# Kernel optimization log

Hardware: AMD Instinct MI355X
Metric: run time of the kernel (lower is better)

The kernel has to match this reference:

```python
import jax, jax.numpy as jnp
import numpy as np
from jax import lax

B, TX, TY = 32, 512, 1024
D, H, FN, KS, L = 256, 2, 1024, 9, 4
WORD_NUM = 256
NEG = -1e9


def sinusoid_table(seq_len, d):
    pos = np.arange(seq_len)[:, None].astype(np.float64)
    i = np.arange(d)[None, :]
    angle = pos / np.power(10000.0, 2 * (i // 2) / d)
    table = np.zeros((seq_len, d))
    table[:, 0::2] = np.sin(angle[:, 0::2])
    table[:, 1::2] = np.cos(angle[:, 1::2])
    return jnp.asarray(table, dtype=jnp.float32)


def setup_inputs():
    key = jax.random.key(0)
    ks = jax.random.split(key, 16)
    s = 0.02
    w = lambda k, shape: jax.random.normal(k, shape, jnp.float32) * s
    embed = w(ks[4], (WORD_NUM, D)).at[0].set(0.0)  # padding_idx=0
    return dict(
        tokens=jax.random.randint(ks[0], (B, TX), 1, WORD_NUM),
        src_lengths=jax.random.randint(ks[1], (B,), TX // 2, TX + 1),
        mel_lengths=jax.random.randint(ks[2], (B,), TY // 2, TY + 1),
        value=jax.random.normal(ks[3], (B, TX, TY), jnp.float32),
        embed=embed,
        pos_enc=sinusoid_table(TX, D),
        wq=w(ks[5], (L, D, D)), bq=jnp.zeros((L, D), jnp.float32),
        wk=w(ks[6], (L, D, D)), bk=jnp.zeros((L, D), jnp.float32),
        wv=w(ks[7], (L, D, D)), bv=jnp.zeros((L, D), jnp.float32),
        wo=w(ks[8], (L, D, D)), bo=jnp.zeros((L, D), jnp.float32),
        ln1_g=jnp.ones((L, D), jnp.float32), ln1_b=jnp.zeros((L, D), jnp.float32),
        c1_w=w(ks[9], (L, FN, D, KS)), c1_b=jnp.zeros((L, FN), jnp.float32),
        c2_w=w(ks[10], (L, D, FN, KS)), c2_b=jnp.zeros((L, D), jnp.float32),
        ln2_g=jnp.ones((L, D), jnp.float32), ln2_b=jnp.zeros((L, D), jnp.float32),
    )


def layer_norm(x, g, b, eps=1e-5):
    m = jnp.mean(x, axis=-1, keepdims=True)
    v = jnp.mean(jnp.square(x - m), axis=-1, keepdims=True)
    return (x - m) * lax.rsqrt(v + eps) * g + b


def conv1d(x, w, b):
    # x: [B, C_in, T], w: [C_out, C_in, K]
    p = (w.shape[-1] - 1) // 2
    y = lax.conv_general_dilated(x, w, (1,), [(p, p)],
                                 dimension_numbers=('NCH', 'OIH', 'NCH'))
    return y + b[None, :, None]


def maximum_path(value, mask):
    # Monotonic alignment search DP. value, mask: [B, Tx, Ty]
    b, tx, ty = value.shape
    value = value * mask
    x_range = jnp.arange(tx)[None, :]

    def fwd_step(v, inp):
        j, val_j = inp
        v0 = jnp.concatenate([jnp.full((b, 1), NEG, value.dtype), v[:, :-1]], axis=1)
        max_mask = v >= v0
        v_max = jnp.where(max_mask, v, v0)
        v_new = jnp.where(x_range <= j, v_max + val_j, NEG)
        return v_new, max_mask

    _, directions = lax.scan(fwd_step, jnp.zeros((b, tx), value.dtype),
                             (jnp.arange(ty), jnp.moveaxis(value, 2, 0)))
    directions = jnp.where(jnp.moveaxis(mask, 2, 0).astype(bool), directions, True)

    idx0 = mask[:, :, 0].sum(1).astype(jnp.int32) - 1  # last valid x index per batch
    brange = jnp.arange(b)

    def bwd_step(idx, dir_j):
        col = jax.nn.one_hot(idx, tx, dtype=value.dtype)
        idx_new = idx + dir_j[brange, idx].astype(jnp.int32) - 1
        return idx_new, col

    _, cols = lax.scan(bwd_step, idx0, directions, reverse=True)
    path = jnp.moveaxis(cols, 0, 2) * mask  # [B, Tx, Ty]
    return path


def reference(tokens, src_lengths, mel_lengths, value, embed, pos_enc,
              wq, bq, wk, bk, wv, bv, wo, bo, ln1_g, ln1_b,
              c1_w, c1_b, c2_w, c2_b, ln2_g, ln2_b):
    bsz, tx = tokens.shape
    pad = jnp.arange(tx)[None, :] >= src_lengths[:, None]      # [B,Tx] True=pad
    mel_pad = jnp.arange(TY)[None, :] >= mel_lengths[:, None]  # [B,Ty]
    dk = D // H
    scale = 1.0 / np.sqrt(dk).astype(np.float32)

    x = embed[tokens] + pos_enc[None, :tx, :]
    for l in range(L):
        # --- multi-head self-attention ---
        res = x
        q = (x @ wq[l] + bq[l]).reshape(bsz, tx, H, dk)
        k = (x @ wk[l] + bk[l]).reshape(bsz, tx, H, dk)
        v = (x @ wv[l] + bv[l]).reshape(bsz, tx, H, dk)
        attn = jnp.einsum('bqhd,bkhd->bhqk', q, k) * scale
        attn = jnp.where(pad[:, None, None, :], NEG, attn)
        attn = jax.nn.softmax(attn, axis=-1)
        out = jnp.einsum('bhqk,bkhd->bqhd', attn, v).reshape(bsz, tx, D)
        x = layer_norm(out @ wo[l] + bo[l] + res, ln1_g[l], ln1_b[l])
        x = jnp.where(pad[:, :, None], 0.0, x)
        # --- conv1d FFN ---
        res = x
        h = x.transpose(0, 2, 1)
        h = jax.nn.relu(conv1d(h, c1_w[l], c1_b[l]))
        h = conv1d(h, c2_w[l], c2_b[l]).transpose(0, 2, 1)
        x = layer_norm(h + res, ln2_g[l], ln2_b[l])
        x = jnp.where(pad[:, :, None], 0.0, x)

    mas_mask = ((~pad)[:, :, None] & (~mel_pad)[:, None, :]).astype(jnp.float32)
    path = maximum_path(value, mas_mask)                 # [B,Tx,Ty]
    expanded = jnp.einsum('bxy,bxd->byd', path, x)       # [B,Ty,D]
    return expanded
```

## Files before the change

kernel.cpp:

```cpp
#include <hip/hip_runtime.h>

#define B_  32
#define TX  512
#define TY  1024
#define D_  256
#define H_  2
#define DK  128
#define FN  1024
#define NL  4
#define TXP 520
#define NEGF (-1e9f)

typedef __attribute__((ext_vector_type(4))) float f32x4;
typedef __attribute__((ext_vector_type(8))) short short8;
typedef __attribute__((ext_vector_type(4))) unsigned short ushort4v;

typedef __attribute__((address_space(3))) unsigned int lds_u32;
typedef __attribute__((address_space(1))) const unsigned int glb_u32;

__device__ __forceinline__ unsigned short f2bf(float x) {
  unsigned int u = __builtin_bit_cast(unsigned int, x);
  u += 0x7fffu + ((u >> 16) & 1u);
  return (unsigned short)(u >> 16);
}
__device__ __forceinline__ float bf2f(unsigned short x) {
  unsigned int u = ((unsigned int)x) << 16;
  return __builtin_bit_cast(float, u);
}
__device__ __forceinline__ void store_bf16x4(unsigned short* p, f32x4 v) {
  ushort4v o; o[0]=f2bf(v[0]); o[1]=f2bf(v[1]); o[2]=f2bf(v[2]); o[3]=f2bf(v[3]);
  *(ushort4v*)p = o;
}
__device__ __forceinline__ float wsum(float v) {
#pragma unroll
  for (int i = 1; i < 64; i <<= 1) v += __shfl_xor(v, i, 64);
  return v;
}
__device__ __forceinline__ float wmax(float v) {
#pragma unroll
  for (int i = 1; i < 64; i <<= 1) v = fmaxf(v, __shfl_xor(v, i, 64));
  return v;
}
__device__ __forceinline__ void gl_lds16(const unsigned short* g, unsigned short* l) {
  __builtin_amdgcn_global_load_lds((glb_u32*)g, (lds_u32*)l, 16, 0, 0);
}
__device__ __forceinline__ float lane_shr1(float x) {
  int r = __builtin_amdgcn_update_dpp(0, __builtin_bit_cast(int, x), 0x138, 0xF, 0xF, false);
  return __builtin_bit_cast(float, r);
}

static const size_t OFF_XB   = 0;
static const size_t SZ_XB    = (size_t)B_*TXP*D_*2;
static const size_t OFF_HB   = OFF_XB + SZ_XB;
static const size_t SZ_HB    = (size_t)B_*TXP*FN*2;
static const size_t OFF_QKV  = OFF_HB + SZ_HB;
static const size_t SZ_QKV   = (size_t)B_*TX*768*2;
static const size_t OFF_S    = OFF_QKV + SZ_QKV;
static const size_t SZ_S     = (size_t)B_*H_*TX*TX*2;
static const size_t OFF_AO   = OFF_S + SZ_S;
static const size_t SZ_AO    = (size_t)B_*TX*D_*2;
static const size_t OFF_T1   = OFF_AO + SZ_AO;
static const size_t SZ_T1    = (size_t)B_*TX*D_*4;
static const size_t OFF_WQKV = OFF_T1 + SZ_T1;
static const size_t SZ_WQKV  = (size_t)NL*768*256*2;
static const size_t OFF_BQKV = OFF_WQKV + SZ_WQKV;
static const size_t SZ_BQKV  = (size_t)NL*768*4;
static const size_t OFF_WO   = OFF_BQKV + SZ_BQKV;
static const size_t SZ_WO    = (size_t)NL*256*256*2;
static const size_t OFF_WT1  = OFF_WO + SZ_WO;
static const size_t SZ_WT1   = (size_t)NL*9*1024*256*2;
static const size_t OFF_WT2  = OFF_WT1 + SZ_WT1;
static const size_t SZ_WT2   = SZ_WT1;
static const size_t OFF_DIRS = OFF_WT2 + SZ_WT2;
static const size_t SZ_DIRS  = (size_t)B_*TY*64;
static const size_t OFF_IDX  = OFF_DIRS + SZ_DIRS;

__global__ void repack_qkvw(const float* __restrict__ wq, const float* __restrict__ wk,
                            const float* __restrict__ wv, unsigned short* __restrict__ out) {
  int i = blockIdx.x*256 + threadIdx.x;
  if (i >= NL*768*256) return;
  int c = i & 255, j = (i >> 8) % 768, l = i / (768*256);
  const float* src = (j < 256) ? wq : (j < 512) ? wk : wv;
  out[i] = f2bf(src[((size_t)l*256 + c)*256 + (j & 255)]);
}
__global__ void repack_bias(const float* __restrict__ bq, const float* __restrict__ bk,
                            const float* __restrict__ bv, float* __restrict__ out) {
  int i = blockIdx.x*256 + threadIdx.x;
  if (i >= NL*768) return;
  int j = i % 768, l = i / 768;
  const float* src = (j < 256) ? bq : (j < 512) ? bk : bv;
  out[i] = src[l*256 + (j & 255)];
}
__global__ void repack_wo(const float* __restrict__ wo, unsigned short* __restrict__ out) {
  int i = blockIdx.x*256 + threadIdx.x;
  if (i >= NL*256*256) return;
  int c = i & 255, j = (i >> 8) & 255, l = i >> 16;
  out[i] = f2bf(wo[((size_t)l*256 + c)*256 + j]);
}
__global__ void repack_c1(const float* __restrict__ w, unsigned short* __restrict__ out) {
  int i = blockIdx.x*256 + threadIdx.x;
  if (i >= NL*9*1024*256) return;
  int c = i & 255; int rest = i >> 8;
  int f = rest & 1023; int rest2 = rest >> 10;
  int k = rest2 % 9, l = rest2 / 9;
  out[i] = f2bf(w[(((size_t)l*1024 + f)*256 + c)*9 + k]);
}
__global__ void repack_c2(const float* __restrict__ w, unsigned short* __restrict__ out) {
  int i = blockIdx.x*256 + threadIdx.x;
  if (i >= NL*9*256*1024) return;
  int f = i & 1023; int rest = i >> 10;
  int d = rest & 255; int rest2 = rest >> 8;
  int k = rest2 % 9, l = rest2 / 9;
  out[i] = f2bf(w[(((size_t)l*256 + d)*1024 + f)*9 + k]);
}
__global__ void zero_halo(unsigned short* __restrict__ xb, unsigned short* __restrict__ hb) {
  int i = blockIdx.x*256 + threadIdx.x;
  if (i < 65536) {
    int b = i >> 11, r = (i >> 8) & 7, c = i & 255;
    int row = (r < 4) ? r : (512 + r);
    xb[((size_t)b*TXP + row)*256 + c] = 0;
  } else {
    int j = i - 65536;
    if (j < 262144) {
      int b = j >> 13, r = (j >> 10) & 7, c = j & 1023;
      int row = (r < 4) ? r : (512 + r);
      hb[((size_t)b*TXP + row)*1024 + c] = 0;
    }
  }
}

__global__ __launch_bounds__(256) void embed_kernel(const int* __restrict__ tok,
    const float* __restrict__ emb, const float* __restrict__ pos,
    unsigned short* __restrict__ xbo ) {
  int row = blockIdx.x*4 + (threadIdx.x >> 6);
  int t = row & 511, b = row >> 9;
  int lane = threadIdx.x & 63;
  int tk = tok[row];
  f32x4 e = *(const f32x4*)(emb + (size_t)tk*256 + lane*4);
  f32x4 p = *(const f32x4*)(pos + (size_t)t*256 + lane*4);
  f32x4 v;
#pragma unroll
  for (int i = 0; i < 4; i++) v[i] = e[i] + p[i];
  store_bf16x4(xbo + ((size_t)b*TXP + t)*256 + lane*4, v);
}

__global__ __launch_bounds__(256) void gemm_mfma(
    const unsigned short* __restrict__ A, long long AbO, long long AhO, int Astr,
    const unsigned short* __restrict__ W, long long WbO, long long WhO, int Wstr,
    const float* __restrict__ bias,
    float* __restrict__ O32, long long O32bO, int O32str,
    unsigned short* __restrict__ O16, long long O16bO, long long O16hO, int O16str,
    int Cin, int Cout, int ks, int relu, int H,
    const int* __restrict__ sl, float scale, int maskmode) {
  __shared__ unsigned short As[128*32];
  __shared__ unsigned short Ws[128*32];
  const int tid = threadIdx.x;
  int b, h;
  if (H == 2) { b = blockIdx.z >> 1; h = blockIdx.z & 1; }
  else        { b = blockIdx.z;      h = 0; }
  const int t0 = blockIdx.x * 128;
  const int f0 = blockIdx.y * 128;
  const unsigned short* Ab = A + (size_t)b * AbO + (size_t)h * AhO;
  const unsigned short* Wb = W + (size_t)b * WbO + (size_t)h * WhO;
  const int lane = tid & 63, w = tid >> 6;
  const int wt = (w & 1) << 6, wf = (w >> 1) << 6;
  const int lr = lane & 15, lh = lane >> 4;
  const int r0 = tid >> 2, cg = (tid & 3) << 3;
  f32x4 zed = {0.f, 0.f, 0.f, 0.f};
  f32x4 acc[4][4];
#pragma unroll
  for (int i = 0; i < 4; i++)
#pragma unroll
    for (int j = 0; j < 4; j++) acc[i][j] = zed;

  for (int k = 0; k < ks; ++k) {
    const unsigned short* AkB = Ab + (size_t)(t0 + k) * Astr;
    const unsigned short* WkB = Wb + ((size_t)k * Cout + f0) * Wstr;
    for (int c0 = 0; c0 < Cin; c0 += 32) {
      __syncthreads();
      gl_lds16(AkB + (size_t)r0 * Astr + (c0 + cg),        As + (size_t)tid * 8);
      gl_lds16(AkB + (size_t)(r0 + 64) * Astr + (c0 + cg), As + (size_t)(tid + 256) * 8);
      gl_lds16(WkB + (size_t)r0 * Wstr + (c0 + cg),        Ws + (size_t)tid * 8);
      gl_lds16(WkB + (size_t)(r0 + 64) * Wstr + (c0 + cg), Ws + (size_t)(tid + 256) * 8);
      __syncthreads();
      short8 af[4], bfv[4];
#pragma unroll
      for (int mt = 0; mt < 4; mt++) af[mt]  = *(const short8*)&As[(wt + mt*16 + lr)*32 + lh*8];
#pragma unroll
      for (int nt = 0; nt < 4; nt++) bfv[nt] = *(const short8*)&Ws[(wf + nt*16 + lr)*32 + lh*8];
#pragma unroll
      for (int mt = 0; mt < 4; mt++)
#pragma unroll
        for (int nt = 0; nt < 4; nt++)
          acc[mt][nt] = __builtin_amdgcn_mfma_f32_16x16x32_bf16(af[mt], bfv[nt], acc[mt][nt], 0, 0, 0);
    }
  }
  const int slb = maskmode ? sl[b] : 0;
#pragma unroll
  for (int mt = 0; mt < 4; mt++) {
    int trow = t0 + wt + mt*16 + lh*4;
#pragma unroll
    for (int nt = 0; nt < 4; nt++) {
      int f = f0 + wf + nt*16 + lr;
      float bb = (!maskmode && bias) ? bias[f] : 0.f;
#pragma unroll
      for (int r = 0; r < 4; r++) {
        float v;
        if (maskmode) {
          v = acc[mt][nt][r] * scale;
          if (f >= slb) v = NEGF;
        } else {
          v = acc[mt][nt][r] + bb;
          if (relu) v = fmaxf(v, 0.f);
        }
        if (O32) O32[(size_t)b*O32bO + (size_t)(trow + r)*O32str + f] = v;
        if (O16) O16[(size_t)b*O16bO + (size_t)h*O16hO + (size_t)(trow + r)*O16str + f] = f2bf(v);
      }
    }
  }
}

__global__ __launch_bounds__(256) void vtrans_kernel(const unsigned short* __restrict__ qkv,
    unsigned short* __restrict__ VT) {
  const int z = blockIdx.z, b = z >> 1, h = z & 1;
  const int t0 = blockIdx.x << 5, d0 = blockIdx.y << 5;
  __shared__ unsigned short tile[32][33];
  const int tx = threadIdx.x, ty = threadIdx.y;
  const unsigned short* src = qkv + (size_t)b*TX*768 + 512 + h*DK;
#pragma unroll
  for (int i = 0; i < 4; i++)
    tile[ty + i*8][tx] = src[(size_t)(t0 + ty + i*8)*768 + d0 + tx];
  __syncthreads();
#pragma unroll
  for (int i = 0; i < 4; i++)
    VT[((size_t)z*DK + d0 + ty + i*8)*512 + t0 + tx] = tile[tx][ty + i*8];
}

__global__ __launch_bounds__(256) void softmax_kernel(unsigned short* __restrict__ S) {
  const int row = blockIdx.x*4 + (threadIdx.x >> 6);
  const int lane = threadIdx.x & 63;
  unsigned short* p = S + (size_t)row*512 + lane*8;
  short8 raw = *(const short8*)p;
  float a[8];
#pragma unroll
  for (int i = 0; i < 8; i++) a[i] = bf2f((unsigned short)raw[i]);
  float m = a[0];
#pragma unroll
  for (int i = 1; i < 8; i++) m = fmaxf(m, a[i]);
  m = wmax(m);
  float s = 0.f;
#pragma unroll
  for (int i = 0; i < 8; i++) { a[i] = __expf(a[i]-m); s += a[i]; }
  s = wsum(s);
  float inv = 1.f / s;
  short8 o;
#pragma unroll
  for (int i = 0; i < 8; i++) o[i] = (short)f2bf(a[i] * inv);
  *(short8*)p = o;
}

__global__ __launch_bounds__(256) void ln_kernel(const float* __restrict__ tin,
    const float* __restrict__ g, const float* __restrict__ bt, const int* __restrict__ sl,
    unsigned short* __restrict__ xbo ) {
  const int row = blockIdx.x*4 + (threadIdx.x >> 6);
  const int b = row >> 9, t = row & 511;
  const int lane = threadIdx.x & 63;
  unsigned short* xp = xbo + ((size_t)b*TXP + t)*256 + lane*4;
  f32x4 tv = *(const f32x4*)(tin + (size_t)row*256 + lane*4);
  ushort4v rv4 = *(const ushort4v*)xp;
  f32x4 s; float su = 0.f, sq = 0.f;
#pragma unroll
  for (int i = 0; i < 4; i++) {
    s[i] = tv[i] + bf2f(rv4[i]);
    su += s[i]; sq += s[i]*s[i];
  }
  su = wsum(su); sq = wsum(sq);
  float mean = su * (1.f/256.f);
  float var = fmaxf(sq * (1.f/256.f) - mean*mean, 0.f);
  float rs = rsqrtf(var + 1e-5f);
  f32x4 gg = *(const f32x4*)(g + lane*4);
  f32x4 bb = *(const f32x4*)(bt + lane*4);
  bool padr = (t >= sl[b]);
  f32x4 y;
#pragma unroll
  for (int i = 0; i < 4; i++) {
    float yy = (s[i]-mean)*rs*gg[i] + bb[i];
    y[i] = padr ? 0.f : yy;
  }
  store_bf16x4(xp, y);
}

__global__ __launch_bounds__(256) void transpose_mask(const float* __restrict__ value,
    const int* __restrict__ sl, const int* __restrict__ ml, float* __restrict__ vT) {
  const int b = blockIdx.z;
  const int x0 = blockIdx.y << 5, y0 = blockIdx.x << 5;
  __shared__ float tile[32][33];
  const int tx = threadIdx.x, ty = threadIdx.y;
  const int slb = sl[b], mlb = ml[b];
#pragma unroll
  for (int i = 0; i < 4; i++) {
    int x = x0 + ty + i*8, y = y0 + tx;
    float v = value[((size_t)b*TX + x)*TY + y];
    tile[ty + i*8][tx] = (x < slb && y < mlb) ? v : 0.f;
  }
  __syncthreads();
#pragma unroll
  for (int i = 0; i < 4; i++) {
    int y = y0 + ty + i*8, x = x0 + tx;
    vT[((size_t)b*TY + y)*TX + x] = tile[tx][ty + i*8];
  }
}

__global__ __launch_bounds__(64, 1) void dp_forward(const float* __restrict__ vT,
    const int* __restrict__ sl, const int* __restrict__ ml, unsigned char* __restrict__ dirs) {
  const int b = blockIdx.x;
  const int lane = threadIdx.x;
  const int slb = sl[b], mlb = ml[b];
  const float* vb = vT + (size_t)b*TY*TX + lane*8;
  unsigned char* db = dirs + (size_t)b*TY*64 + lane;
  const int xbase = lane*8;
  float v[8];
#pragma unroll
  for (int i = 0; i < 8; i++) v[i] = 0.f;
  f32x4 b0[8][2], b1[8][2], b2[8][2];
  auto load8 = [&](int jb, f32x4 (&bf)[8][2]) {
#pragma unroll
    for (int u = 0; u < 8; u++) {
      const float* p = vb + (size_t)(jb*8 + u)*TX;
      bf[u][0] = *(const f32x4*)p;
      bf[u][1] = *(const f32x4*)(p + 4);
    }
  };
  auto comp8 = [&](int jb, f32x4 (&bf)[8][2]) {
#pragma unroll
    for (int u = 0; u < 8; u++) {
      const int j = jb*8 + u;
      float vp = lane_shr1(v[7]);
      if (lane == 0) vp = NEGF;
      float v0[8];
      v0[0] = vp;
#pragma unroll
      for (int i = 1; i < 8; i++) v0[i] = v[i-1];
      unsigned int byt = 0;
#pragma unroll
      for (int i = 0; i < 8; i++) {
        const int x = xbase + i;
        bool ge = (v[i] >= v0[i]);
        bool dbit = (x < slb) ? ge : true;
        byt |= ((unsigned)dbit) << i;
        float vm = fmaxf(v[i], v0[i]);
        float val = (i < 4) ? bf[u][0][i] : bf[u][1][i-4];
        v[i] = (x <= j) ? (vm + val) : NEGF;
      }
      if (j < mlb) db[(size_t)j*64] = (unsigned char)byt;
    }
  };
  const int jbEnd = (mlb + 7) >> 3;
  load8(0, b0);
  __builtin_amdgcn_sched_barrier(0);
  load8(1, b1);
  __builtin_amdgcn_sched_barrier(0);
  load8(2, b2);
  __builtin_amdgcn_sched_barrier(0);
  for (int jb = 0; jb < jbEnd; jb += 3) {
    comp8(jb, b0);
    __builtin_amdgcn_sched_barrier(0);
    if (jb + 3 < jbEnd) { load8(jb + 3, b0); }
    __builtin_amdgcn_sched_barrier(0);
    if (jb + 1 < jbEnd) {
      comp8(jb + 1, b1);
      __builtin_amdgcn_sched_barrier(0);
      if (jb + 4 < jbEnd) { load8(jb + 4, b1); }
      __builtin_amdgcn_sched_barrier(0);
    }
    if (jb + 2 < jbEnd) {
      comp8(jb + 2, b2);
      __builtin_amdgcn_sched_barrier(0);
      if (jb + 5 < jbEnd) { load8(jb + 5, b2); }
      __builtin_amdgcn_sched_barrier(0);
    }
  }
}

__global__ __launch_bounds__(64) void dp_backward(const unsigned char* __restrict__ dirs,
    const int* __restrict__ sl, const int* __restrict__ ml, int* __restrict__ idxout) {
  extern __shared__ unsigned int ldsw[];
  const int b = blockIdx.x, lane = threadIdx.x;
  const unsigned int* src = (const unsigned int*)(dirs + (size_t)b*TY*64);
  for (int i = lane; i < TY*16; i += 64) ldsw[i] = src[i];
  __syncthreads();
  if (lane == 0) {
    int idx = sl[b] - 1;
    const int mlb = ml[b];
    int* ob = idxout + b*TY;
    for (int j = TY - 1; j >= 0; --j) {
      if (j < mlb) {
        ob[j] = idx;
        unsigned int w = ldsw[j*16 + (idx >> 5)];
        idx += (int)((w >> (idx & 31)) & 1u) - 1;
      } else ob[j] = -1;
    }
  }
}

__global__ __launch_bounds__(256) void gather_kernel(const unsigned short* __restrict__ xbo,
    const int* __restrict__ idxout, float* __restrict__ out) {
  const int row = blockIdx.x*4 + (threadIdx.x >> 6);
  const int lane = threadIdx.x & 63;
  const int b = row >> 10;
  const int idx = idxout[row];
  f32x4 v;
  if (idx >= 0) {
    ushort4v r = *(const ushort4v*)(xbo + ((size_t)b*TXP + idx)*256 + lane*4);
#pragma unroll
    for (int i = 0; i < 4; i++) v[i] = bf2f(r[i]);
  } else { v[0]=0.f; v[1]=0.f; v[2]=0.f; v[3]=0.f; }
  *(f32x4*)(out + (size_t)row*256 + lane*4) = v;
}

extern "C" void kernel_launch(void* const* d_in, const int* in_sizes, int n_in,
                              void* d_out, int out_size, void* d_ws, size_t ws_size,
                              hipStream_t stream) {
  const int*   tokens = (const int*)d_in[0];
  const int*   sl     = (const int*)d_in[1];
  const int*   ml     = (const int*)d_in[2];
  const float* value  = (const float*)d_in[3];
  const float* emb    = (const float*)d_in[4];
  const float* pos    = (const float*)d_in[5];
  const float* wq     = (const float*)d_in[6];
  const float* bq     = (const float*)d_in[7];
  const float* wk     = (const float*)d_in[8];
  const float* bk     = (const float*)d_in[9];
  const float* wv     = (const float*)d_in[10];
  const float* bv     = (const float*)d_in[11];
  const float* wo     = (const float*)d_in[12];
  const float* bo     = (const float*)d_in[13];
  const float* ln1g   = (const float*)d_in[14];
  const float* ln1bb  = (const float*)d_in[15];
  const float* c1w    = (const float*)d_in[16];
  const float* c1b    = (const float*)d_in[17];
  const float* c2w    = (const float*)d_in[18];
  const float* c2b    = (const float*)d_in[19];
  const float* ln2g   = (const float*)d_in[20];
  const float* ln2bb  = (const float*)d_in[21];

  char* w8 = (char*)d_ws;
  unsigned short* xb     = (unsigned short*)(w8 + OFF_XB);
  unsigned short* hb     = (unsigned short*)(w8 + OFF_HB);
  unsigned short* qkvb   = (unsigned short*)(w8 + OFF_QKV);
  unsigned short* S      = (unsigned short*)(w8 + OFF_S);
  float*          vT     = (float*)(w8 + OFF_HB);
  unsigned short* VT     = (unsigned short*)(w8 + OFF_T1);
  unsigned short* ao     = (unsigned short*)(w8 + OFF_AO);
  float*          T1     = (float*)(w8 + OFF_T1);
  unsigned short* wqkv_r = (unsigned short*)(w8 + OFF_WQKV);
  float*          bqkv   = (float*)(w8 + OFF_BQKV);
  unsigned short* wo_r   = (unsigned short*)(w8 + OFF_WO);
  unsigned short* wt1r   = (unsigned short*)(w8 + OFF_WT1);
  unsigned short* wt2r   = (unsigned short*)(w8 + OFF_WT2);
  unsigned char*  dirs   = (unsigned char*)(w8 + OFF_DIRS);
  int*            idxout = (int*)(w8 + OFF_IDX);
  float*          out    = (float*)d_out;

  const float scale = 0.08838834764831843f;

  repack_qkvw<<<(NL*768*256 + 255)/256, 256, 0, stream>>>(wq, wk, wv, wqkv_r);
  repack_bias<<<(NL*768 + 255)/256, 256, 0, stream>>>(bq, bk, bv, bqkv);
  repack_wo<<<(NL*256*256 + 255)/256, 256, 0, stream>>>(wo, wo_r);
  repack_c1<<<(NL*9*1024*256 + 255)/256, 256, 0, stream>>>(c1w, wt1r);
  repack_c2<<<(NL*9*256*1024 + 255)/256, 256, 0, stream>>>(c2w, wt2r);

  transpose_mask<<<dim3(32, 16, 32), dim3(32, 8), 0, stream>>>(value, sl, ml, vT);
  dp_forward<<<32, 64, 0, stream>>>(vT, sl, ml, dirs);
  dp_backward<<<32, 64, 65536, stream>>>(dirs, sl, ml, idxout);

  zero_halo<<<(327680 + 255)/256, 256, 0, stream>>>(xb, hb);
  embed_kernel<<<4096, 256, 0, stream>>>(tokens, emb, pos, xb + 4*256);

  for (int l = 0; l < NL; l++) {
    gemm_mfma<<<dim3(4, 6, 32), 256, 0, stream>>>(
        xb + 4*256, (long long)TXP*256, 0, 256,
        wqkv_r + (size_t)l*768*256, 0, 0, 256,
        bqkv + l*768,
        nullptr, 0, 0,
        qkvb, (long long)TX*768, 0, 768,
        256, 768, 1, 0, 1, nullptr, 0.f, 0);
    gemm_mfma<<<dim3(4, 4, 64), 256, 0, stream>>>(
        qkvb, (long long)TX*768, 128, 768,
        qkvb + 256, (long long)TX*768, 128, 768,
        nullptr,
        nullptr, 0, 0,
        S, (long long)2*512*512, (long long)512*512, 512,
        128, 512, 1, 0, 2, sl, scale, 1);
    softmax_kernel<<<8192, 256, 0, stream>>>(S);
    vtrans_kernel<<<dim3(16, 4, 64), dim3(32, 8), 0, stream>>>(qkvb, VT);
    gemm_mfma<<<dim3(4, 1, 64), 256, 0, stream>>>(
        S, (long long)2*512*512, (long long)512*512, 512,
        VT, (long long)2*DK*512, (long long)DK*512, 512,
        nullptr,
        nullptr, 0, 0,
        ao, (long long)TX*256, 128, 256,
        512, 128, 1, 0, 2, nullptr, 0.f, 0);
    gemm_mfma<<<dim3(4, 2, 32), 256, 0, stream>>>(
        ao, (long long)TX*256, 0, 256,
        wo_r + (size_t)l*256*256, 0, 0, 256,
        bo + l*256,
        T1, (long long)TX*256, 256,
        nullptr, 0, 0, 0,
        256, 256, 1, 0, 1, nullptr, 0.f, 0);
    ln_kernel<<<4096, 256, 0, stream>>>(T1, ln1g + l*256, ln1bb + l*256, sl, xb + 4*256);
    gemm_mfma<<<dim3(4, 8, 32), 256, 0, stream>>>(
        xb, (long long)TXP*256, 0, 256,
        wt1r + (size_t)l*9*1024*256, 0, 0, 256,
        c1b + l*1024,
        nullptr, 0, 0,
        hb + 4*1024, (long long)TXP*1024, 0, 1024,
        256, 1024, 9, 1, 1, nullptr, 0.f, 0);
    gemm_mfma<<<dim3(4, 2, 32), 256, 0, stream>>>(
        hb, (long long)TXP*1024, 0, 1024,
        wt2r + (size_t)l*9*256*1024, 0, 0, 1024,
        c2b + l*256,
        T1, (long long)TX*256, 256,
        nullptr, 0, 0, 0,
        1024, 256, 9, 0, 1, nullptr, 0.f, 0);
    ln_kernel<<<4096, 256, 0, stream>>>(T1, ln2g + l*256, ln2bb + l*256, sl, xb + 4*256);
  }

  gather_kernel<<<8192, 256, 0, stream>>>(xb + 4*256, idxout, out);
  (void)in_sizes; (void)n_in; (void)out_size; (void)ws_size;
}
```

Before: 2.299 ms.

## Fuse DP forward/backward in LDS and reuse A tile across conv taps

The GEMM loop order is swapped so the activation tile (with an 8-row halo) is loaded once per channel chunk and reused across all conv taps. Weight tiles are double-buffered per tap, cutting global loads and barriers for the conv FFN. The monotonic alignment DP forward and backward passes are merged into one kernel. It stages values into LDS with async global-to-LDS loads and keeps the direction bits in LDS instead of global memory. The backtrace is unrolled to prefetch direction bytes, which adds complexity in waitcnt handling and in the LDS budget.

```diff
diff --git a/kernel.cpp b/kernel.cpp
--- a/kernel.cpp
+++ b/kernel.cpp
@@ -42,6 +42,9 @@
   return v;
 }
 __device__ __forceinline__ void gl_lds16(const unsigned short* g, unsigned short* l) {
+  __builtin_amdgcn_global_load_lds((glb_u32*)g, (lds_u32*)l, 16, 0, 0);
+}
+__device__ __forceinline__ void gl_lds16f(const float* g, float* l) {
   __builtin_amdgcn_global_load_lds((glb_u32*)g, (lds_u32*)l, 16, 0, 0);
 }
 __device__ __forceinline__ float lane_shr1(float x) {
@@ -152,8 +155,8 @@
     unsigned short* __restrict__ O16, long long O16bO, long long O16hO, int O16str,
     int Cin, int Cout, int ks, int relu, int H,
     const int* __restrict__ sl, float scale, int maskmode) {
-  __shared__ unsigned short As[128*32];
-  __shared__ unsigned short Ws[128*32];
+  __shared__ unsigned short As[136*32];
+  __shared__ unsigned short Ws[2*128*32];
   const int tid = threadIdx.x;
   int b, h;
   if (H == 2) { b = blockIdx.z >> 1; h = blockIdx.z & 1; }
@@ -173,21 +176,31 @@
 #pragma unroll
     for (int j = 0; j < 4; j++) acc[i][j] = zed;
 
-  for (int k = 0; k < ks; ++k) {
-    const unsigned short* AkB = Ab + (size_t)(t0 + k) * Astr;
-    const unsigned short* WkB = Wb + ((size_t)k * Cout + f0) * Wstr;
-    for (int c0 = 0; c0 < Cin; c0 += 32) {
+  for (int c0 = 0; c0 < Cin; c0 += 32) {
+    __syncthreads();
+    gl_lds16(Ab + (size_t)(t0 + r0) * Astr + (c0 + cg),         As + (size_t)tid * 8);
+    gl_lds16(Ab + (size_t)(t0 + r0 + 64) * Astr + (c0 + cg),    As + (size_t)(tid + 256) * 8);
+    if (ks > 1 && tid < 32)
+      gl_lds16(Ab + (size_t)(t0 + r0 + 128) * Astr + (c0 + cg), As + (size_t)(tid + 512) * 8);
+    {
+      const unsigned short* W0 = Wb + (size_t)f0 * Wstr;
+      gl_lds16(W0 + (size_t)r0 * Wstr + (c0 + cg),        Ws + (size_t)tid * 8);
+      gl_lds16(W0 + (size_t)(r0 + 64) * Wstr + (c0 + cg), Ws + (size_t)(tid + 256) * 8);
+    }
+    for (int k = 0; k < ks; ++k) {
       __syncthreads();
-      gl_lds16(AkB + (size_t)r0 * Astr + (c0 + cg),        As + (size_t)tid * 8);
-      gl_lds16(AkB + (size_t)(r0 + 64) * Astr + (c0 + cg), As + (size_t)(tid + 256) * 8);
-      gl_lds16(WkB + (size_t)r0 * Wstr + (c0 + cg),        Ws + (size_t)tid * 8);
-      gl_lds16(WkB + (size_t)(r0 + 64) * Wstr + (c0 + cg), Ws + (size_t)(tid + 256) * 8);
-      __syncthreads();
+      if (k + 1 < ks) {
+        const unsigned short* Wn = Wb + ((size_t)(k + 1) * Cout + f0) * Wstr;
+        unsigned short* Wd = Ws + (size_t)((k + 1) & 1) * 4096;
+        gl_lds16(Wn + (size_t)r0 * Wstr + (c0 + cg),        Wd + (size_t)tid * 8);
+        gl_lds16(Wn + (size_t)(r0 + 64) * Wstr + (c0 + cg), Wd + (size_t)(tid + 256) * 8);
+      }
+      const unsigned short* Wsk = Ws + (size_t)(k & 1) * 4096;
       short8 af[4], bfv[4];
 #pragma unroll
-      for (int mt = 0; mt < 4; mt++) af[mt]  = *(const short8*)&As[(wt + mt*16 + lr)*32 + lh*8];
-#pragma unroll
-      for (int nt = 0; nt < 4; nt++) bfv[nt] = *(const short8*)&Ws[(wf + nt*16 + lr)*32 + lh*8];
+      for (int mt = 0; mt < 4; mt++) af[mt]  = *(const short8*)&As[(k + wt + mt*16 + lr)*32 + lh*8];
+#pragma unroll
+      for (int nt = 0; nt < 4; nt++) bfv[nt] = *(const short8*)&Wsk[(wf + nt*16 + lr)*32 + lh*8];
 #pragma unroll
       for (int mt = 0; mt < 4; mt++)
 #pragma unroll
@@ -311,94 +324,123 @@
   }
 }
 
-__global__ __launch_bounds__(64, 1) void dp_forward(const float* __restrict__ vT,
-    const int* __restrict__ sl, const int* __restrict__ ml, unsigned char* __restrict__ dirs) {
-  const int b = blockIdx.x;
-  const int lane = threadIdx.x;
+template<bool RAMP>
+__device__ __forceinline__ void dp_comp8(
+    int jb, const float* valbuf, unsigned long long* dll,
+    float v[8], int lane, int xbase, unsigned int vmask, unsigned int fmask,
+    bool lane0) {
+  unsigned int w0 = 0, w1 = 0;
+#pragma unroll
+  for (int u = 0; u < 8; ++u) {
+    const int j = jb*8 + u;
+    f32x4 a0 = *(const f32x4*)(valbuf + u*512 + lane*8);
+    f32x4 a1 = *(const f32x4*)(valbuf + u*512 + lane*8 + 4);
+    float vp = lane_shr1(v[7]);
+    if (lane0) vp = NEGF;
+    unsigned int ge = 0;
+#pragma unroll
+    for (int i = 7; i >= 1; --i) {
+      unsigned int g = (v[i] >= v[i-1]) ? 1u : 0u;
+      ge = (ge << 1) | g;
+      float nv = fmaxf(v[i], v[i-1]) + ((i < 4) ? a0[i] : a1[i-4]);
+      if (RAMP) v[i] = (xbase + i <= j) ? nv : NEGF;
+      else      v[i] = nv;
+    }
+    {
+      unsigned int g = (v[0] >= vp) ? 1u : 0u;
+      ge = (ge << 1) | g;
+      float nv = fmaxf(v[0], vp) + a0[0];
+      if (RAMP) v[0] = (xbase <= j) ? nv : NEGF;
+      else      v[0] = nv;
+    }
+    unsigned int byt = (ge & vmask) | fmask;
+    if (u < 4) w0 |= byt << (8*u); else w1 |= byt << (8*(u-4));
+  }
+  dll[jb*64 + lane] = ((unsigned long long)w1 << 32) | w0;
+}
+
+__global__ __launch_bounds__(64, 1) void dp_fused(const float* __restrict__ vT,
+    const int* __restrict__ sl, const int* __restrict__ ml,
+    int* __restrict__ idxout) {
+  __shared__ float sval[3*4096];
+  __shared__ unsigned long long dll[TY*8];
+  unsigned char* dld = (unsigned char*)dll;
+  const int b = blockIdx.x, lane = threadIdx.x;
   const int slb = sl[b], mlb = ml[b];
-  const float* vb = vT + (size_t)b*TY*TX + lane*8;
-  unsigned char* db = dirs + (size_t)b*TY*64 + lane;
+  const float* vb = vT + (size_t)b*TY*TX;
   const int xbase = lane*8;
+  const bool lane0 = (lane == 0);
+  unsigned int vmaskv = 0;
+#pragma unroll
+  for (int i = 0; i < 8; ++i) if (xbase + i < slb) vmaskv |= (1u << i);
+  const unsigned int fmaskv = (~vmaskv) & 0xffu;
   float v[8];
 #pragma unroll
-  for (int i = 0; i < 8; i++) v[i] = 0.f;
-  f32x4 b0[8][2], b1[8][2], b2[8][2];
-  auto load8 = [&](int jb, f32x4 (&bf)[8][2]) {
-#pragma unroll
-    for (int u = 0; u < 8; u++) {
-      const float* p = vb + (size_t)(jb*8 + u)*TX;
-      bf[u][0] = *(const f32x4*)p;
-      bf[u][1] = *(const f32x4*)(p + 4);
+  for (int i = 0; i < 8; ++i) v[i] = 0.f;
+  const int jbEnd = (mlb + 7) >> 3;
+
+  auto stage = [&](int jb, float* buf) {
+    const float* src = vb + (size_t)jb*8*TX;
+#pragma unroll
+    for (int u = 0; u < 8; ++u) {
+      gl_lds16f(src + u*TX + lane*4,       buf + u*512);
+      gl_lds16f(src + u*TX + 256 + lane*4, buf + u*512 + 256);
     }
   };
-  auto comp8 = [&](int jb, f32x4 (&bf)[8][2]) {
-#pragma unroll
-    for (int u = 0; u < 8; u++) {
-      const int j = jb*8 + u;
-      float vp = lane_shr1(v[7]);
-      if (lane == 0) vp = NEGF;
-      float v0[8];
-      v0[0] = vp;
-#pragma unroll
-      for (int i = 1; i < 8; i++) v0[i] = v[i-1];
-      unsigned int byt = 0;
-#pragma unroll
-      for (int i = 0; i < 8; i++) {
-        const int x = xbase + i;
-        bool ge = (v[i] >= v0[i]);
-        bool dbit = (x < slb) ? ge : true;
-        byt |= ((unsigned)dbit) << i;
-        float vm = fmaxf(v[i], v0[i]);
-        float val = (i < 4) ? bf[u][0][i] : bf[u][1][i-4];
-        v[i] = (x <= j) ? (vm + val) : NEGF;
+  stage(0, sval);
+  stage(1, sval + 4096);
+  stage(2, sval + 8192);
+  int buf = 0;
+  int jb = 0;
+  for (; jb < 64; ++jb) {
+    if (jb + 2 < jbEnd)      asm volatile("s_waitcnt vmcnt(32)" ::: "memory");
+    else if (jb + 1 < jbEnd) asm volatile("s_waitcnt vmcnt(16)" ::: "memory");
+    else                     asm volatile("s_waitcnt vmcnt(0)"  ::: "memory");
+    float* vbuf = sval + buf*4096;
+    dp_comp8<true>(jb, vbuf, dll, v, lane, xbase, vmaskv, fmaskv, lane0);
+    __builtin_amdgcn_sched_barrier(0);
+    if (jb + 3 < jbEnd) stage(jb + 3, vbuf);
+    buf = (buf == 2) ? 0 : buf + 1;
+  }
+  for (; jb < jbEnd; ++jb) {
+    if (jb + 2 < jbEnd)      asm volatile("s_waitcnt vmcnt(32)" ::: "memory");
+    else if (jb + 1 < jbEnd) asm volatile("s_waitcnt vmcnt(16)" ::: "memory");
+    else                     asm volatile("s_waitcnt vmcnt(0)"  ::: "memory");
+    float* vbuf = sval + buf*4096;
+    dp_comp8<false>(jb, vbuf, dll, v, lane, xbase, vmaskv, fmaskv, lane0);
+    __builtin_amdgcn_sched_barrier(0);
+    if (jb + 3 < jbEnd) stage(jb + 3, vbuf);
+    buf = (buf == 2) ? 0 : buf + 1;
+  }
+  for (int jj = mlb + lane; jj < TY; jj += 64) idxout[b*TY + jj] = -1;
+  if (lane0) {
+    int* ob = idxout + b*TY;
+    int idx = slb - 1;
+    int j = mlb - 1;
+    while (j >= 6) {
+      int o0 = idx >> 3;
+      int o1 = (o0 > 0) ? (o0 - 1) : 0;
+      unsigned int bc[7], ba[7];
+#pragma unroll
+      for (int s = 0; s < 7; ++s) {
+        int r = j - s;
+        int rbase = ((r >> 3) << 9) + (r & 7);
+        bc[s] = dld[rbase + o0*8];
+        ba[s] = dld[rbase + o1*8];
       }
-      if (j < mlb) db[(size_t)j*64] = (unsigned char)byt;
-    }
-  };
-  const int jbEnd = (mlb + 7) >> 3;
-  load8(0, b0);
-  __builtin_amdgcn_sched_barrier(0);
-  load8(1, b1);
-  __builtin_amdgcn_sched_barrier(0);
-  load8(2, b2);
-  __builtin_amdgcn_sched_barrier(0);
-  for (int jb = 0; jb < jbEnd; jb += 3) {
-    comp8(jb, b0);
-    __builtin_amdgcn_sched_barrier(0);
-    if (jb + 3 < jbEnd) { load8(jb + 3, b0); }
-    __builtin_amdgcn_sched_barrier(0);
-    if (jb + 1 < jbEnd) {
-      comp8(jb + 1, b1);
-      __builtin_amdgcn_sched_barrier(0);
-      if (jb + 4 < jbEnd) { load8(jb + 4, b1); }
-      __builtin_amdgcn_sched_barrier(0);
-    }
-    if (jb + 2 < jbEnd) {
-      comp8(jb + 2, b2);
-      __builtin_amdgcn_sched_barrier(0);
-      if (jb + 5 < jbEnd) { load8(jb + 5, b2); }
-      __builtin_amdgcn_sched_barrier(0);
-    }
-  }
-}
-
-__global__ __launch_bounds__(64) void dp_backward(const unsigned char* __restrict__ dirs,
-    const int* __restrict__ sl, const int* __restrict__ ml, int* __restrict__ idxout) {
-  extern __shared__ unsigned int ldsw[];
-  const int b = blockIdx.x, lane = threadIdx.x;
-  const unsigned int* src = (const unsigned int*)(dirs + (size_t)b*TY*64);
-  for (int i = lane; i < TY*16; i += 64) ldsw[i] = src[i];
-  __syncthreads();
-  if (lane == 0) {
-    int idx = sl[b] - 1;
-    const int mlb = ml[b];
-    int* ob = idxout + b*TY;
-    for (int j = TY - 1; j >= 0; --j) {
-      if (j < mlb) {
-        ob[j] = idx;
-        unsigned int w = ldsw[j*16 + (idx >> 5)];
-        idx += (int)((w >> (idx & 31)) & 1u) - 1;
-      } else ob[j] = -1;
+#pragma unroll
+      for (int s = 0; s < 7; ++s) {
+        ob[j - s] = idx;
+        unsigned int byt = ((idx >> 3) == o0) ? bc[s] : ba[s];
+        idx += (int)((byt >> (idx & 7)) & 1u) - 1;
+      }
+      j -= 7;
+    }
+    while (j >= 0) {
+      ob[j] = idx;
+      unsigned int byt = dld[((j >> 3) << 9) + (j & 7) + (idx >> 3)*8];
+      idx += (int)((byt >> (idx & 7)) & 1u) - 1;
+      --j;
     }
   }
 }
@@ -458,7 +500,6 @@
   unsigned short* wo_r   = (unsigned short*)(w8 + OFF_WO);
   unsigned short* wt1r   = (unsigned short*)(w8 + OFF_WT1);
   unsigned short* wt2r   = (unsigned short*)(w8 + OFF_WT2);
-  unsigned char*  dirs   = (unsigned char*)(w8 + OFF_DIRS);
   int*            idxout = (int*)(w8 + OFF_IDX);
   float*          out    = (float*)d_out;
 
@@ -471,8 +512,7 @@
   repack_c2<<<(NL*9*256*1024 + 255)/256, 256, 0, stream>>>(c2w, wt2r);
 
   transpose_mask<<<dim3(32, 16, 32), dim3(32, 8), 0, stream>>>(value, sl, ml, vT);
-  dp_forward<<<32, 64, 0, stream>>>(vT, sl, ml, dirs);
-  dp_backward<<<32, 64, 65536, stream>>>(dirs, sl, ml, idxout);
+  dp_fused<<<32, 64, 0, stream>>>(vT, sl, ml, idxout);
 
   zero_halo<<<(327680 + 255)/256, 256, 0, stream>>>(xb, hb);
   embed_kernel<<<4096, 256, 0, stream>>>(tokens, emb, pos, xb + 4*256);
```

Measured after the change: 2.050 ms. 10.8% less time.
